# Performance work log

Hardware: AMD Instinct MI355X
Metric: run time of the kernel (lower is better)

## Reference

```python
import jax, jax.numpy as jnp
import numpy as np

B, L, D_MODEL, H, D_K, D_V = 64, 52, 4096, 32, 128, 128
NEW_C = D_MODEL // H  # per-head input channel after the (faithful) raw reshape


def setup_inputs() -> dict:
    key = jax.random.key(0)
    ks = jax.random.split(key, 12)
    s = 0.02
    return {
        "Q": jax.random.normal(ks[0], (B, L, D_MODEL), jnp.float32),
        "K": jax.random.normal(ks[1], (B, L, D_MODEL), jnp.float32),
        "V": jax.random.normal(ks[2], (B, L, D_MODEL), jnp.float32),
        "Wq": jax.random.normal(ks[3], (H, NEW_C, D_K), jnp.float32) * s,
        "bq": jnp.zeros((H, D_K), jnp.float32),
        "Wk": jax.random.normal(ks[4], (H, NEW_C, D_K), jnp.float32) * s,
        "bk": jnp.zeros((H, D_K), jnp.float32),
        "Wv": jax.random.normal(ks[5], (H, NEW_C, D_V), jnp.float32) * s,
        "bv": jnp.zeros((H, D_V), jnp.float32),
        "Wo": jax.random.normal(ks[6], (H * D_V, D_MODEL), jnp.float32) * s,
        "bo": jnp.zeros((D_MODEL,), jnp.float32),
    }


def reference(Q, K, V, Wq, bq, Wk, bk, Wv, bv, Wo, bo):
    # Faithful to source: raw reshape (B, L, D) -> (B, H, L, D/H), NOT a channel split.
    def split(x):
        return x.reshape(B, H, L, NEW_C)

    q = jnp.einsum('bhlc,hck->bhlk', split(Q), Wq) + bq[None, :, None, :]  # (B,H,L,D_K)
    k = jnp.einsum('bhlc,hck->bhlk', split(K), Wk) + bk[None, :, None, :]
    v = jnp.einsum('bhlc,hcv->bhlv', split(V), Wv) + bv[None, :, None, :]

    scores = jnp.einsum('bhqk,bhmk->bhqm', q, k) / jnp.sqrt(jnp.asarray(D_K, q.dtype))
    # causal mask: keep j <= i, else -inf (matches the numpy masking loop)
    causal = jnp.tril(jnp.ones((L, L), bool))
    scores = jnp.where(causal[None, None], scores, -jnp.inf)
    attn = jax.nn.softmax(scores, axis=-1)
    o = jnp.einsum('bhqm,bhmv->bhqv', attn, v)  # (B,H,L,D_V)
    o = o.transpose(0, 2, 1, 3).reshape(B, L, H * D_V)  # concat heads on last axis
    # Dropout(0.1) is identity at inference.
    return o @ Wo + bo
```

## Files before the change

kernel.cpp:

```cpp
#include <hip/hip_runtime.h>
#include <hip/hip_bf16.h>

#define B_SZ   64
#define L_SZ   52
#define DMODEL 4096
#define H_SZ   32
#define C_SZ   128
#define DK     128

#define GM 3328
#define GN 4096
#define GK 4096

typedef __bf16 bf16x8 __attribute__((ext_vector_type(8)));
typedef float  f32x4  __attribute__((ext_vector_type(4)));

__device__ __forceinline__ void gload_lds16(const void* g, void* l) {
  __builtin_amdgcn_global_load_lds(
      (__attribute__((address_space(1))) void*)(void*)g,
      (__attribute__((address_space(3))) void*)l, 16, 0, 0);
}

__global__ __launch_bounds__(256) void wo_transpose_kernel(
    const float* __restrict__ Wo, __hip_bfloat16* __restrict__ WoT) {
  __shared__ float tile[64][65];
  const int nt = blockIdx.x, mt = blockIdx.y;
  const int t = threadIdx.x;
  const int r  = t >> 4;
  const int c4 = (t & 15) << 2;
#pragma unroll
  for (int p = 0; p < 4; ++p) {
    const int rr = r + p * 16;
    const float4 v = *(const float4*)(Wo + (size_t)(mt * 64 + rr) * 4096 + nt * 64 + c4);
    tile[rr][c4 + 0] = v.x; tile[rr][c4 + 1] = v.y;
    tile[rr][c4 + 2] = v.z; tile[rr][c4 + 3] = v.w;
  }
  __syncthreads();
#pragma unroll
  for (int p = 0; p < 4; ++p) {
    const int rr = r + p * 16;
    union { __hip_bfloat16 h[4]; ushort4 u; } o4;
#pragma unroll
    for (int e = 0; e < 4; ++e) o4.h[e] = __float2bfloat16(tile[c4 + e][rr]);
    *(ushort4*)(WoT + (size_t)(nt * 64 + rr) * 4096 + mt * 64 + c4) = o4.u;
  }
}

__global__ __launch_bounds__(256) void w3_transpose_kernel(
    const float* __restrict__ Wq, const float* __restrict__ Wk,
    const float* __restrict__ Wv, __hip_bfloat16* __restrict__ WqT,
    __hip_bfloat16* __restrict__ WkT, __hip_bfloat16* __restrict__ WvT) {
  __shared__ float tile[64][65];
  const int bz = blockIdx.z;
  const float* in = (bz < 32 ? Wq : (bz < 64 ? Wk : Wv)) + (size_t)(bz & 31) * 16384;
  __hip_bfloat16* out = (bz < 32 ? WqT : (bz < 64 ? WkT : WvT)) + (size_t)(bz & 31) * 16384;
  const int nt = blockIdx.x, mt = blockIdx.y;
  const int t = threadIdx.x;
  const int r  = t >> 4;
  const int c4 = (t & 15) << 2;
#pragma unroll
  for (int p = 0; p < 4; ++p) {
    const int rr = r + p * 16;
    const float4 v = *(const float4*)(in + (size_t)(mt * 64 + rr) * 128 + nt * 64 + c4);
    tile[rr][c4 + 0] = v.x; tile[rr][c4 + 1] = v.y;
    tile[rr][c4 + 2] = v.z; tile[rr][c4 + 3] = v.w;
  }
  __syncthreads();
#pragma unroll
  for (int p = 0; p < 4; ++p) {
    const int rr = r + p * 16;
    union { __hip_bfloat16 h[4]; ushort4 u; } o4;
#pragma unroll
    for (int e = 0; e < 4; ++e) o4.h[e] = __float2bfloat16(tile[c4 + e][rr]);
    *(ushort4*)(out + (size_t)(nt * 64 + rr) * 128 + mt * 64 + c4) = o4.u;
  }
}

template <bool TRANSPOSED>
__device__ __forceinline__ void wave_proj(
    const __hip_bfloat16* __restrict__ xs, const __hip_bfloat16* __restrict__ WT,
    const float* __restrict__ bias, __hip_bfloat16* __restrict__ out,
    int n0, int r16, int kq) {
  f32x4 acc[4][2] = {};
  bf16x8 bfrag[2][4];
#pragma unroll
  for (int nt = 0; nt < 2; ++nt)
#pragma unroll
    for (int kk = 0; kk < 4; ++kk)
      bfrag[nt][kk] = *(const bf16x8*)(WT + (n0 + nt * 16 + r16) * 128 + kk * 32 + kq * 8);
#pragma unroll
  for (int kk = 0; kk < 4; ++kk) {
    bf16x8 a[4];
#pragma unroll
    for (int mt = 0; mt < 4; ++mt)
      a[mt] = *(const bf16x8*)(xs + (mt * 16 + r16) * 136 + kk * 32 + kq * 8);
#pragma unroll
    for (int mt = 0; mt < 4; ++mt)
#pragma unroll
      for (int nt = 0; nt < 2; ++nt)
        acc[mt][nt] = __builtin_amdgcn_mfma_f32_16x16x32_bf16(a[mt], bfrag[nt][kk], acc[mt][nt], 0, 0, 0);
  }
#pragma unroll
  for (int nt = 0; nt < 2; ++nt) {
    const int col = n0 + nt * 16 + r16;
    const float bv = bias[col];
#pragma unroll
    for (int mt = 0; mt < 4; ++mt) {
      const int m0 = mt * 16 + kq * 4;
      if (!TRANSPOSED) {
#pragma unroll
        for (int i = 0; i < 4; ++i)
          out[(m0 + i) * 136 + col] = __float2bfloat16(acc[mt][nt][i] + bv);
      } else {
        union { __hip_bfloat16 h[4]; ushort4 u; } o4;
        if (m0 < 52) {
#pragma unroll
          for (int i = 0; i < 4; ++i) o4.h[i] = __float2bfloat16(acc[mt][nt][i] + bv);
        } else {
          o4.u = make_ushort4(0, 0, 0, 0);
        }
        *(ushort4*)(out + col * 72 + m0) = o4.u;
      }
    }
  }
}

__global__ __launch_bounds__(256, 2) void attn_kernel(
    const float* __restrict__ Qin, const float* __restrict__ Kin,
    const float* __restrict__ Vin,
    const __hip_bfloat16* __restrict__ WqT, const float* __restrict__ bq,
    const __hip_bfloat16* __restrict__ WkT, const float* __restrict__ bk,
    const __hip_bfloat16* __restrict__ WvT, const float* __restrict__ bv,
    __hip_bfloat16* __restrict__ Oc) {
  __shared__ __align__(16) char lds[70656];
  __hip_bfloat16* xs0  = (__hip_bfloat16*)(lds);
  __hip_bfloat16* xs1  = (__hip_bfloat16*)(lds + 17408);
  __hip_bfloat16* xs2  = (__hip_bfloat16*)(lds + 34816);
  __hip_bfloat16* vT   = (__hip_bfloat16*)(lds + 52224);
  __hip_bfloat16* q_sh = (__hip_bfloat16*)(lds + 34816);
  __hip_bfloat16* k_sh = (__hip_bfloat16*)(lds);
  float*          s_sh = (float*)(lds + 17408);
  __hip_bfloat16* p_sh = (__hip_bfloat16*)(lds + 34816);

  const int h = blockIdx.x, bb = blockIdx.y;
  const int t = threadIdx.x;
  const int w = t >> 6, lane = t & 63;
  const int r16 = lane & 15, kq = lane >> 4;
  const size_t xoff = (size_t)bb * (L_SZ * DMODEL) + (size_t)h * (L_SZ * C_SZ);

  {
    const float* xp[3] = {Qin + xoff, Kin + xoff, Vin + xoff};
    __hip_bfloat16* xd[3] = {xs0, xs1, xs2};
#pragma unroll
    for (int tz = 0; tz < 3; ++tz) {
      const float* X = xp[tz];
      __hip_bfloat16* xs = xd[tz];
      for (int idx = t; idx < 52 * 32; idx += 256) {
        const int row = idx >> 5, c4 = (idx & 31) << 2;
        const float4 v = *(const float4*)(X + row * 128 + c4);
        union { __hip_bfloat16 h[4]; ushort4 u; } o4;
        o4.h[0] = __float2bfloat16(v.x); o4.h[1] = __float2bfloat16(v.y);
        o4.h[2] = __float2bfloat16(v.z); o4.h[3] = __float2bfloat16(v.w);
        *(ushort4*)(xs + row * 136 + c4) = o4.u;
      }
      if (t < 12 * 17) {
        const int row = 52 + t / 17, c8 = (t % 17) * 8;
        *(uint4*)(xs + row * 136 + c8) = make_uint4(0, 0, 0, 0);
      }
    }
  }
  __syncthreads();

  wave_proj<true>(xs2, WvT + (size_t)h * 16384, bv + h * 128, vT, w * 32, r16, kq);
  __syncthreads();
  wave_proj<false>(xs0, WqT + (size_t)h * 16384, bq + h * 128, q_sh, w * 32, r16, kq);
  __syncthreads();
  wave_proj<false>(xs1, WkT + (size_t)h * 16384, bk + h * 128, k_sh, w * 32, r16, kq);
  __syncthreads();

  {
    const int n0 = w * 16;
    f32x4 sacc[4] = {};
#pragma unroll
    for (int kk = 0; kk < 4; ++kk) {
      const bf16x8 bf_ = *(const bf16x8*)(k_sh + (n0 + r16) * 136 + kk * 32 + kq * 8);
#pragma unroll
      for (int mt = 0; mt < 4; ++mt) {
        const bf16x8 a = *(const bf16x8*)(q_sh + (mt * 16 + r16) * 136 + kk * 32 + kq * 8);
        sacc[mt] = __builtin_amdgcn_mfma_f32_16x16x32_bf16(a, bf_, sacc[mt], 0, 0, 0);
      }
    }
    const float scale = 0.08838834764831845f;
#pragma unroll
    for (int mt = 0; mt < 4; ++mt)
#pragma unroll
      for (int i = 0; i < 4; ++i)
        s_sh[(mt * 16 + kq * 4 + i) * 68 + n0 + r16] = sacc[mt][i] * scale;
  }
  __syncthreads();

  {
    const int r = t >> 2, qd = t & 3;
    if (r < 52) {
      float v[16];
      float mx = -3e38f;
#pragma unroll
      for (int j4 = 0; j4 < 4; ++j4) {
        const f32x4 s4 = *(const f32x4*)(s_sh + r * 68 + qd * 16 + j4 * 4);
#pragma unroll
        for (int e = 0; e < 4; ++e) {
          const int col = qd * 16 + j4 * 4 + e;
          const float val = (col <= r) ? s4[e] : -3e38f;
          v[j4 * 4 + e] = val;
          mx = fmaxf(mx, val);
        }
      }
      mx = fmaxf(mx, __shfl_xor(mx, 1));
      mx = fmaxf(mx, __shfl_xor(mx, 2));
      float ex[16];
      float sum = 0.f;
#pragma unroll
      for (int j = 0; j < 16; ++j) {
        const int col = qd * 16 + j;
        const float e = (col <= r) ? __expf(v[j] - mx) : 0.f;
        ex[j] = e; sum += e;
      }
      sum += __shfl_xor(sum, 1);
      sum += __shfl_xor(sum, 2);
      const float inv = 1.0f / sum;
      union { __hip_bfloat16 h[8]; uint4 q; } p0, p1;
#pragma unroll
      for (int j = 0; j < 8; ++j) {
        p0.h[j] = __float2bfloat16(ex[j] * inv);
        p1.h[j] = __float2bfloat16(ex[8 + j] * inv);
      }
      *(uint4*)(p_sh + r * 72 + qd * 16)     = p0.q;
      *(uint4*)(p_sh + r * 72 + qd * 16 + 8) = p1.q;
    } else {
      *(uint4*)(p_sh + r * 72 + qd * 16)     = make_uint4(0, 0, 0, 0);
      *(uint4*)(p_sh + r * 72 + qd * 16 + 8) = make_uint4(0, 0, 0, 0);
    }
  }
  __syncthreads();

  {
    const int n0 = w * 32;
    f32x4 oacc[4][2] = {};
#pragma unroll
    for (int kk = 0; kk < 2; ++kk) {
      bf16x8 bfr[2];
#pragma unroll
      for (int nt = 0; nt < 2; ++nt)
        bfr[nt] = *(const bf16x8*)(vT + (n0 + nt * 16 + r16) * 72 + kk * 32 + kq * 8);
#pragma unroll
      for (int mt = 0; mt < 4; ++mt) {
        const bf16x8 a = *(const bf16x8*)(p_sh + (mt * 16 + r16) * 72 + kk * 32 + kq * 8);
#pragma unroll
        for (int nt = 0; nt < 2; ++nt)
          oacc[mt][nt] = __builtin_amdgcn_mfma_f32_16x16x32_bf16(a, bfr[nt], oacc[mt][nt], 0, 0, 0);
      }
    }
    const size_t obase = (size_t)bb * 52 * 4096 + (size_t)h * 128;
#pragma unroll
    for (int nt = 0; nt < 2; ++nt) {
      const int col = n0 + nt * 16 + r16;
#pragma unroll
      for (int mt = 0; mt < 4; ++mt) {
        const int row0 = mt * 16 + kq * 4;
#pragma unroll
        for (int i = 0; i < 4; ++i) {
          const int row = row0 + i;
          if (row < 52)
            Oc[obase + (size_t)row * 4096 + col] = __float2bfloat16(oacc[mt][nt][i]);
        }
      }
    }
  }
}

__global__ __launch_bounds__(512, 2) void out_gemm_kernel(
    const __hip_bfloat16* __restrict__ A, const __hip_bfloat16* __restrict__ Bt,
    const float* __restrict__ bias, float* __restrict__ C) {
  __shared__ __align__(16) char lds[131072];

  int bid = blockIdx.x;
  bid = (bid & 7) * 26 + (bid >> 3);
  const int tm = bid >> 4;
  const int tn = bid & 15;

  const int t = threadIdx.x;
  const int w = t >> 6, lane = t & 63;
  const int wm = w >> 2, wn = w & 3;
  const int r16 = lane & 15, kq = lane >> 4;

  const int srow = (w << 5) + (lane >> 2);
  const int sswz = ((lane & 3) ^ ((srow >> 1) & 3)) << 3;
  const char* gA = (const char*)(A  + (size_t)(tm * 256 + srow) * GK + sswz);
  const char* gB = (const char*)(Bt + (size_t)(tn * 256 + srow) * GK + sswz);
  const int dstA = (w << 11) + (lane << 4);
  const int dstB = 16384 + dstA;

  const int rswz = (kq ^ ((r16 >> 1) & 3)) << 4;
  const int cA = (wm << 13) + r16 * 64 + rswz;
  const int cB = 16384 + (wn << 12) + r16 * 64 + rswz;

  f32x4 acc[8][4] = {};

#pragma unroll
  for (int pt = 0; pt < 3; ++pt) {
    char* db = lds + (pt << 15);
    const int sk = pt << 6;
    gload_lds16(gA + sk,          db + dstA);
    gload_lds16(gA + sk + 131072, db + dstA + 1024);
    gload_lds16(gB + sk,          db + dstB);
    gload_lds16(gB + sk + 131072, db + dstB + 1024);
  }
  asm volatile("s_waitcnt vmcnt(8)" ::: "memory");
  asm volatile("s_barrier" ::: "memory");

#pragma unroll 1
  for (int kt = 0; kt < 128; ++kt) {
    const int st = kt + 3;
    const int sk = (st < 128 ? st : 127) << 6;
    char* db = lds + ((st & 3) << 15);
    gload_lds16(gA + sk,          db + dstA);
    gload_lds16(gA + sk + 131072, db + dstA + 1024);
    gload_lds16(gB + sk,          db + dstB);
    gload_lds16(gB + sk + 131072, db + dstB + 1024);

    const char* rb = lds + ((kt & 3) << 15);
    bf16x8 af[8], bf_[4];
#pragma unroll
    for (int mf = 0; mf < 8; ++mf) af[mf] = *(const bf16x8*)(rb + cA + mf * 1024);
#pragma unroll
    for (int nf = 0; nf < 4; ++nf) bf_[nf] = *(const bf16x8*)(rb + cB + nf * 1024);

    __builtin_amdgcn_s_setprio(1);
#pragma unroll
    for (int mf = 0; mf < 8; ++mf)
#pragma unroll
      for (int nf = 0; nf < 4; ++nf)
        acc[mf][nf] = __builtin_amdgcn_mfma_f32_16x16x32_bf16(af[mf], bf_[nf], acc[mf][nf], 0, 0, 0);
    __builtin_amdgcn_s_setprio(0);

    asm volatile("s_waitcnt vmcnt(8)" ::: "memory");
    asm volatile("s_barrier" ::: "memory");
  }

  const int row0 = tm * 256 + wm * 128 + kq * 4;
  const int col0 = tn * 256 + wn * 64 + r16;
#pragma unroll
  for (int nf = 0; nf < 4; ++nf) {
    const int col = col0 + nf * 16;
    const float bv = bias[col];
#pragma unroll
    for (int mf = 0; mf < 8; ++mf) {
      const int row = row0 + mf * 16;
#pragma unroll
      for (int i = 0; i < 4; ++i)
        C[(size_t)(row + i) * GN + col] = acc[mf][nf][i] + bv;
    }
  }
}

extern "C" void kernel_launch(void* const* d_in, const int* in_sizes, int n_in,
                              void* d_out, int out_size, void* d_ws, size_t ws_size,
                              hipStream_t stream) {
  const float* Q  = (const float*)d_in[0];
  const float* K  = (const float*)d_in[1];
  const float* V  = (const float*)d_in[2];
  const float* Wq = (const float*)d_in[3];
  const float* bq = (const float*)d_in[4];
  const float* Wk = (const float*)d_in[5];
  const float* bk = (const float*)d_in[6];
  const float* Wv = (const float*)d_in[7];
  const float* bv = (const float*)d_in[8];
  const float* Wo = (const float*)d_in[9];
  const float* bo = (const float*)d_in[10];
  float* out = (float*)d_out;

  char* wsb = (char*)d_ws;
  __hip_bfloat16* WoT = (__hip_bfloat16*)wsb;
  __hip_bfloat16* Oc  = (__hip_bfloat16*)(wsb + (size_t)GN * GK * 2);
  __hip_bfloat16* WqT = (__hip_bfloat16*)(wsb + (size_t)GN * GK * 2 + (size_t)GM * GN * 2);
  __hip_bfloat16* WkT = WqT + (size_t)H_SZ * C_SZ * DK;
  __hip_bfloat16* WvT = WkT + (size_t)H_SZ * C_SZ * DK;

  w3_transpose_kernel<<<dim3(2, 2, 96), 256, 0, stream>>>(Wq, Wk, Wv, WqT, WkT, WvT);
  wo_transpose_kernel<<<dim3(64, 64), 256, 0, stream>>>(Wo, WoT);
  attn_kernel<<<dim3(H_SZ, B_SZ), 256, 0, stream>>>(Q, K, V, WqT, bq, WkT, bk, WvT, bv, Oc);
  out_gemm_kernel<<<dim3(13 * 16), 512, 0, stream>>>(Oc, WoT, bo, out);
}
```

Measured before the change: 220.1 us.

## Restructure output GEMM pipeline into double-buffered 128-K tiles with phased loads

Reworks the output projection GEMM main loop from a 4-stage, 64-wide K pipeline into a double-buffered loop over 128-wide K tiles, split into four compute phases. Each phase interleaves part of the next tiles' global-to-LDS loads with a half of the MFMA work, with barriers between phases. The aim is to overlap memory traffic with compute more evenly and halve the loop iterations. It adds more barriers per iteration and relies on careful vmcnt accounting, and reuses the current read buffer for loads two stages ahead, which risks hazards if the waits are wrong.

```diff
diff --git a/kernel.cpp b/kernel.cpp
--- a/kernel.cpp
+++ b/kernel.cpp
@@ -278,6 +278,40 @@
   }
 }
 
+#define STAGE(GBASE, REGOFF, KT, KS, WB) do {                                  \
+    const __hip_bfloat16* s_ = (GBASE) + (size_t)(KT) * 64 + (KS) * 32;        \
+    char* d_ = (WB) + (REGOFF) + ((KS) ? 16384 : 0) + t * 16;                  \
+    gload_lds16(s_, d_);                                                       \
+    gload_lds16(s_ + (size_t)128 * GK, d_ + 8192);                             \
+  } while (0)
+
+#define PHASE(KS, MH, STAGE_STMT, EXTRA_WAIT)                                  \
+  {                                                                            \
+    bf16x8 af[4];                                                              \
+    _Pragma("unroll")                                                          \
+    for (int mf = 0; mf < 4; ++mf)                                             \
+      af[mf] = *(const bf16x8*)(rb + (KS) * 16384 + aBase + ((MH) * 4 + mf) * 1024); \
+    if ((MH) == 0) {                                                           \
+      _Pragma("unroll")                                                        \
+      for (int nf = 0; nf < 4; ++nf)                                           \
+        bf[nf] = *(const bf16x8*)(rb + 32768 + (KS) * 16384 + bBase + nf * 1024); \
+    }                                                                          \
+    STAGE_STMT;                                                                \
+    __builtin_amdgcn_s_barrier();                                              \
+    asm volatile("s_waitcnt lgkmcnt(0)" ::: "memory");                         \
+    __builtin_amdgcn_sched_barrier(0);                                         \
+    __builtin_amdgcn_s_setprio(1);                                             \
+    _Pragma("unroll")                                                          \
+    for (int mf = 0; mf < 4; ++mf)                                             \
+      _Pragma("unroll")                                                        \
+      for (int nf = 0; nf < 4; ++nf)                                           \
+        acc[(MH) * 4 + mf][nf] = __builtin_amdgcn_mfma_f32_16x16x32_bf16(      \
+            af[mf], bf[nf], acc[(MH) * 4 + mf][nf], 0, 0, 0);                  \
+    __builtin_amdgcn_s_setprio(0);                                             \
+    EXTRA_WAIT;                                                                \
+    __builtin_amdgcn_s_barrier();                                              \
+  }
+
 __global__ __launch_bounds__(512, 2) void out_gemm_kernel(
     const __hip_bfloat16* __restrict__ A, const __hip_bfloat16* __restrict__ Bt,
     const float* __restrict__ bias, float* __restrict__ C) {
@@ -293,59 +327,41 @@
   const int wm = w >> 2, wn = w & 3;
   const int r16 = lane & 15, kq = lane >> 4;
 
-  const int srow = (w << 5) + (lane >> 2);
-  const int sswz = ((lane & 3) ^ ((srow >> 1) & 3)) << 3;
-  const char* gA = (const char*)(A  + (size_t)(tm * 256 + srow) * GK + sswz);
-  const char* gB = (const char*)(Bt + (size_t)(tn * 256 + srow) * GK + sswz);
-  const int dstA = (w << 11) + (lane << 4);
-  const int dstB = 16384 + dstA;
-
-  const int rswz = (kq ^ ((r16 >> 1) & 3)) << 4;
-  const int cA = (wm << 13) + r16 * 64 + rswz;
-  const int cB = 16384 + (wn << 12) + r16 * 64 + rswz;
+  const int srow = t >> 2;
+  const int sgslot = (t & 3) ^ ((srow >> 1) & 3);
+  const __hip_bfloat16* gA0 = A  + (size_t)(tm * 256 + srow) * GK + sgslot * 8;
+  const __hip_bfloat16* gB0 = Bt + (size_t)(tn * 256 + srow) * GK + sgslot * 8;
+
+  const int slotr = kq ^ ((r16 >> 1) & 3);
+  const int aBase = (wm * 128 + r16) * 64 + slotr * 16;
+  const int bBase = (wn * 64 + r16) * 64 + slotr * 16;
 
   f32x4 acc[8][4] = {};
 
-#pragma unroll
-  for (int pt = 0; pt < 3; ++pt) {
-    char* db = lds + (pt << 15);
-    const int sk = pt << 6;
-    gload_lds16(gA + sk,          db + dstA);
-    gload_lds16(gA + sk + 131072, db + dstA + 1024);
-    gload_lds16(gB + sk,          db + dstB);
-    gload_lds16(gB + sk + 131072, db + dstB + 1024);
-  }
-  asm volatile("s_waitcnt vmcnt(8)" ::: "memory");
-  asm volatile("s_barrier" ::: "memory");
+  STAGE(gA0, 0,     0, 0, lds);
+  STAGE(gB0, 32768, 0, 0, lds);
+  STAGE(gA0, 0,     0, 1, lds);
+  STAGE(gB0, 32768, 0, 1, lds);
+  STAGE(gA0, 0,     1, 0, lds + 65536);
+  STAGE(gB0, 32768, 1, 0, lds + 65536);
+  asm volatile("s_waitcnt vmcnt(4)" ::: "memory");
+  __builtin_amdgcn_s_barrier();
 
 #pragma unroll 1
-  for (int kt = 0; kt < 128; ++kt) {
-    const int st = kt + 3;
-    const int sk = (st < 128 ? st : 127) << 6;
-    char* db = lds + ((st & 3) << 15);
-    gload_lds16(gA + sk,          db + dstA);
-    gload_lds16(gA + sk + 131072, db + dstA + 1024);
-    gload_lds16(gB + sk,          db + dstB);
-    gload_lds16(gB + sk + 131072, db + dstB + 1024);
-
-    const char* rb = lds + ((kt & 3) << 15);
-    bf16x8 af[8], bf_[4];
-#pragma unroll
-    for (int mf = 0; mf < 8; ++mf) af[mf] = *(const bf16x8*)(rb + cA + mf * 1024);
-#pragma unroll
-    for (int nf = 0; nf < 4; ++nf) bf_[nf] = *(const bf16x8*)(rb + cB + nf * 1024);
-
-    __builtin_amdgcn_s_setprio(1);
-#pragma unroll
-    for (int mf = 0; mf < 8; ++mf)
-#pragma unroll
-      for (int nf = 0; nf < 4; ++nf)
-        acc[mf][nf] = __builtin_amdgcn_mfma_f32_16x16x32_bf16(af[mf], bf_[nf], acc[mf][nf], 0, 0, 0);
-    __builtin_amdgcn_s_setprio(0);
-
-    asm volatile("s_waitcnt vmcnt(8)" ::: "memory");
-    asm volatile("s_barrier" ::: "memory");
-  }
+  for (int kt = 0; kt < 64; ++kt) {
+    const char* rb = lds + ((kt & 1) << 16);
+    char* wb1 = lds + (((kt + 1) & 1) << 16);
+    char* wb2 = (char*)rb;
+    const int st1 = kt + 1 < 64 ? kt + 1 : 63;
+    const int st2 = kt + 2 < 64 ? kt + 2 : 63;
+    bf16x8 bf[4];
+    PHASE(0, 0, STAGE(gA0, 0,     st1, 1, wb1), )
+    PHASE(0, 1, STAGE(gB0, 32768, st1, 1, wb1), )
+    PHASE(1, 0, STAGE(gA0, 0,     st2, 0, wb2), )
+    PHASE(1, 1, STAGE(gB0, 32768, st2, 0, wb2),
+          asm volatile("s_waitcnt vmcnt(4)" ::: "memory"))
+  }
+  asm volatile("s_waitcnt vmcnt(0)" ::: "memory");
 
   const int row0 = tm * 256 + wm * 128 + kq * 4;
   const int col0 = tn * 256 + wn * 64 + r16;
```

After: 218.0 us. Within noise of the previous version (-0.9%).
